# Optimization experiments

Hardware: AMD Instinct MI355X
Metric: run time of the kernel (lower is better)

The kernel has to match this reference:

```python
import jax, jax.numpy as jnp
import numpy as np

N_ITERS = 150   # unrolled projected-subgradient iterations of the convex DRO program
LR0 = 0.05      # initial step size (decays as 1/sqrt(k))


def project_simplex(v):
    """Euclidean projection of v onto the probability simplex {z >= 0, sum z = 1}."""
    n = v.shape[0]
    u = jnp.sort(v)[::-1]
    css = jnp.cumsum(u)
    idx = jnp.arange(1, n + 1, dtype=v.dtype)
    rho = jnp.sum(u + (1.0 - css) / idx > 0)
    theta = (css[rho - 1] - 1.0) / rho.astype(v.dtype)
    return jnp.maximum(v - theta, 0.0)


def dro_solve(ep, y_hat, delta, gamma):
    """Solve the TV-DRO portfolio problem (Ben-Tal et al. 2013 tractable dual):
        min_{z in simplex, c, eta, lam>=0}
            eta + delta*lam + (1/T) sum_t max(-lam, (ep_t@z - c)^2 - eta) - gamma * y_hat@z
    via unrolled projected subgradient descent (differentiable solver layer).
    """
    n_obs, n_y = ep.shape

    def objective(params):
        z, c, eta, lam = params
        r = ep @ z - c                       # (n_obs,) residual portfolio returns
        m = jnp.maximum(-lam, r * r - eta)   # TV phi-conjugate term
        return eta + delta * lam + jnp.mean(m) - gamma * jnp.dot(y_hat, z)

    grad_fn = jax.grad(objective)
    init = (jnp.full((n_y,), 1.0 / n_y, dtype=ep.dtype),
            jnp.zeros((), ep.dtype), jnp.zeros((), ep.dtype),
            jnp.asarray(0.1, ep.dtype))

    def step(params, k):
        g = grad_fn(params)
        lr = LR0 / jnp.sqrt(1.0 + k)
        z, c, eta, lam = [p - lr * gi for p, gi in zip(params, g)]
        z = project_simplex(z)
        lam = jnp.maximum(lam, 0.0)
        return (z, c, eta, lam), None

    (z, _, _, _), _ = jax.lax.scan(step, init, jnp.arange(N_ITERS, dtype=ep.dtype))
    return z


def setup_inputs() -> dict:
    key = jax.random.key(0)
    k1, k2, k3, k4 = jax.random.split(key, 4)
    n_obs, n_x, n_y = 256, 64, 128
    X = jax.random.normal(k1, (n_obs, n_x), dtype=jnp.float32)
    Y = 0.05 * jax.random.normal(k2, (n_obs, n_y), dtype=jnp.float32)
    W = jax.random.normal(k3, (n_y, n_x), dtype=jnp.float32) / np.sqrt(n_x)
    b = 0.01 * jax.random.normal(k4, (n_y,), dtype=jnp.float32)
    delta = jnp.asarray(0.1, jnp.float32)
    gamma = jnp.asarray(0.1, jnp.float32)
    return {"X": X, "Y": Y, "W": W, "b": b, "delta": delta, "gamma": gamma}


def reference(X, Y, W, b, delta, gamma):
    Y_hat = X @ W.T + b            # pred_layer applied to each x_t (batched)
    ep = Y - Y_hat                 # (n_obs, n_y) residuals
    # One DRO solve per scenario y_hat_t, all sharing the same residual matrix ep.
    Z_star = jax.vmap(lambda yh: dro_solve(ep, yh, delta, gamma))(Y_hat)
    return Z_star, Y_hat
```

## Files before the change

### kernel.cpp

```cpp
#include <hip/hip_runtime.h>
#include <math.h>

#define T_OBS 256
#define NY 128
#define NITER 150

#define DPP_ROW_SHR1 0x111
#define DPP_ROW_SHR2 0x112
#define DPP_ROW_SHR4 0x114
#define DPP_ROW_SHR8 0x118
#define DPP_BCAST15  0x142
#define DPP_BCAST31  0x143

#define DPP_ADD_F32(x, ctrl) \
    (x) += __int_as_float(__builtin_amdgcn_update_dpp(0, __float_as_int(x), (ctrl), 0xf, 0xf, true))

__device__ __forceinline__ void wave_sum2(float& a, float& b) {
    DPP_ADD_F32(a, DPP_ROW_SHR1); DPP_ADD_F32(b, DPP_ROW_SHR1);
    DPP_ADD_F32(a, DPP_ROW_SHR2); DPP_ADD_F32(b, DPP_ROW_SHR2);
    DPP_ADD_F32(a, DPP_ROW_SHR4); DPP_ADD_F32(b, DPP_ROW_SHR4);
    DPP_ADD_F32(a, DPP_ROW_SHR8); DPP_ADD_F32(b, DPP_ROW_SHR8);
    DPP_ADD_F32(a, DPP_BCAST15);  DPP_ADD_F32(b, DPP_BCAST15);
    DPP_ADD_F32(a, DPP_BCAST31);  DPP_ADD_F32(b, DPP_BCAST31);
    a = __int_as_float(__builtin_amdgcn_readlane(__float_as_int(a), 63));
    b = __int_as_float(__builtin_amdgcn_readlane(__float_as_int(b), 63));
}

__device__ __forceinline__ float rl(float x, int l) {
    return __int_as_float(__builtin_amdgcn_readlane(__float_as_int(x), l));
}

__global__ __launch_bounds__(128)
void pred_kernel(const float* __restrict__ X, const float* __restrict__ Y,
                 const float* __restrict__ W, const float* __restrict__ b,
                 float* __restrict__ yhat, float* __restrict__ ep) {
    __shared__ float xrow[64];
    const int t = blockIdx.x;
    const int j = threadIdx.x;
    if (j < 64) xrow[j] = X[t * 64 + j];
    __syncthreads();
    const float* wr = W + j * 64;
    float acc = 0.f;
#pragma unroll
    for (int x = 0; x < 64; ++x) acc = fmaf(xrow[x], wr[x], acc);
    const float yh = acc + b[j];
    yhat[t * NY + j] = yh;
    ep[t * NY + j] = Y[t * NY + j] - yh;
}

__global__ __launch_bounds__(256, 1)
void dro_kernel(const float* __restrict__ ep_g, const float* __restrict__ yhat_g,
                float* __restrict__ z_out,
                const float* __restrict__ d_delta, const float* __restrict__ d_gamma) {
    __shared__ float gzp[2][4][NY];
    __shared__ __align__(16) float red[2][8];

    const int tid  = threadIdx.x;
    const int lane = tid & 63;
    const int wid  = tid >> 6;
    const int blk  = blockIdx.x;

    float4 rA[32];
    {
        const float4* eg4 = (const float4*)ep_g + tid * 32;
#pragma unroll
        for (int q = 0; q < 32; ++q) rA[q] = eg4[q];
    }

    const int j0    = lane << 1;
    const int tbase = wid << 6;
    float2 rB[64];
#pragma unroll
    for (int tt = 0; tt < 64; ++tt)
        rB[tt] = *(const float2*)(ep_g + (tbase + tt) * NY + j0);

    const float yh0 = yhat_g[blk * NY + j0];
    const float yh1 = yhat_g[blk * NY + j0 + 1];

    float z0 = 1.0f / 128.0f, z1 = 1.0f / 128.0f;
    float act0 = 1.f, act1 = 1.f;

    const float delta = d_delta[0];
    const float gamma = d_gamma[0];
    float c = 0.f, eta = 0.f, lam = 0.1f;
    int buf = 0;

    for (int k = 0; k < NITER; ++k) {
        const float lr = 0.05f * __builtin_amdgcn_rsqf(1.0f + (float)k);

        float a0 = 0.f, a1 = 0.f, a2 = 0.f, a3 = 0.f;
#pragma unroll
        for (int q = 0; q < 32; ++q) {
            const float4 e = rA[q];
            const float za = rl(z0, 2 * q);
            const float zb = rl(z1, 2 * q);
            const float zc = rl(z0, 2 * q + 1);
            const float zd = rl(z1, 2 * q + 1);
            a0 = fmaf(e.x, za, a0);
            a1 = fmaf(e.y, zb, a1);
            a2 = fmaf(e.z, zc, a2);
            a3 = fmaf(e.w, zd, a3);
        }
        const float r  = (a0 + a1) + (a2 + a3) - c;
        const float q2 = r * r - eta;
        const float aa = -lam;
        const float st = (q2 > aa) ? 1.0f : ((q2 == aa) ? 0.5f : 0.0f);
        const float wv = st * r;

        float s1 = st, s2 = wv;
        wave_sum2(s1, s2);
        if (lane == 0) { red[buf][wid * 2] = s1; red[buf][wid * 2 + 1] = s2; }

        float p0 = 0.f, p1 = 0.f, p2 = 0.f, p3 = 0.f;
#pragma unroll
        for (int tt = 0; tt < 64; tt += 2) {
            const float wa = rl(wv, tt);
            const float wb = rl(wv, tt + 1);
            const float2 ea = rB[tt];
            const float2 eb = rB[tt + 1];
            p0 = fmaf(wa, ea.x, p0);
            p1 = fmaf(wa, ea.y, p1);
            p2 = fmaf(wb, eb.x, p2);
            p3 = fmaf(wb, eb.y, p3);
        }
        *(float2*)&gzp[buf][wid][j0] = make_float2(p0 + p2, p1 + p3);

        __syncthreads();

        const float4 rd0 = *(const float4*)&red[buf][0];
        const float4 rd1 = *(const float4*)&red[buf][4];
        const float S1 = (rd0.x + rd0.z) + (rd1.x + rd1.z);
        const float S2 = (rd0.y + rd0.w) + (rd1.y + rd1.w);
        c   -= lr * (-(2.0f / 256.0f) * S2);
        eta -= lr * (1.0f - S1 * (1.0f / 256.0f));
        lam  = fmaxf(lam - lr * (delta - 1.0f + S1 * (1.0f / 256.0f)), 0.0f);

        const float2 g0v = *(const float2*)&gzp[buf][0][j0];
        const float2 g1v = *(const float2*)&gzp[buf][1][j0];
        const float2 g2v = *(const float2*)&gzp[buf][2][j0];
        const float2 g3v = *(const float2*)&gzp[buf][3][j0];
        const float g0 = (g0v.x + g1v.x) + (g2v.x + g3v.x);
        const float g1 = (g0v.y + g1v.y) + (g2v.y + g3v.y);
        const float v0 = z0 - lr * ((2.0f / 256.0f) * g0 - gamma * yh0);
        const float v1 = z1 - lr * ((2.0f / 256.0f) * g1 - gamma * yh1);

        float theta = 0.f;
        for (int attempt = 0; attempt < 2; ++attempt) {
            for (int m = 0; m < 128; ++m) {
                float s  = act0 * v0 + act1 * v1;
                float cc = act0 + act1;
                wave_sum2(s, cc);
                theta = (s - 1.0f) * __builtin_amdgcn_rcpf(cc);
                const float n0 = (v0 > theta) ? act0 : 0.f;
                const float n1 = (v1 > theta) ? act1 : 0.f;
                const bool changed = (n0 != act0) || (n1 != act1);
                act0 = n0; act1 = n1;
                if (!__any(changed)) break;
            }
            const bool viol = ((act0 == 0.f) && (v0 > theta)) ||
                              ((act1 == 0.f) && (v1 > theta));
            if (!__any(viol)) break;
            act0 = 1.f; act1 = 1.f;
        }
        z0 = fmaxf(v0 - theta, 0.f);
        z1 = fmaxf(v1 - theta, 0.f);

        buf ^= 1;
    }

    if (wid == 0) *(float2*)&z_out[blk * NY + j0] = make_float2(z0, z1);
}

extern "C" void kernel_launch(void* const* d_in, const int* in_sizes, int n_in,
                              void* d_out, int out_size, void* d_ws, size_t ws_size,
                              hipStream_t stream) {
    const float* X       = (const float*)d_in[0];
    const float* Y       = (const float*)d_in[1];
    const float* W       = (const float*)d_in[2];
    const float* b       = (const float*)d_in[3];
    const float* d_delta = (const float*)d_in[4];
    const float* d_gamma = (const float*)d_in[5];

    float* z_out    = (float*)d_out;
    float* yhat_out = z_out + T_OBS * NY;
    float* ep_ws    = (float*)d_ws;

    pred_kernel<<<T_OBS, 128, 0, stream>>>(X, Y, W, b, yhat_out, ep_ws);
    dro_kernel<<<T_OBS, 256, 0, stream>>>(ep_ws, yhat_out, z_out, d_delta, d_gamma);
}
```

Measured before the change: 238.7 us.

## Split DRO solve across 512 threads with halved per-thread register tiles

Doubles the DRO block size from 256 to 512 threads. Each observation row's ep@z dot product is split in half across two threads, and the halves are combined through LDS. The gradient reduction over observations now spans 8 waves of 32 rows each, with the redundant wave sums scaled by 0.5. The aim is to halve per-thread serial work and register tiles so more waves run per CU. The cost is an extra __syncthreads per iteration and more LDS traffic, and the simplex projection is now computed redundantly by all 8 waves.

```diff
diff --git a/kernel.cpp b/kernel.cpp
--- a/kernel.cpp
+++ b/kernel.cpp
@@ -48,31 +48,35 @@
     ep[t * NY + j] = Y[t * NY + j] - yh;
 }
 
-__global__ __launch_bounds__(256, 1)
+__global__ __launch_bounds__(512, 2)
 void dro_kernel(const float* __restrict__ ep_g, const float* __restrict__ yhat_g,
                 float* __restrict__ z_out,
                 const float* __restrict__ d_delta, const float* __restrict__ d_gamma) {
-    __shared__ float gzp[2][4][NY];
-    __shared__ __align__(16) float red[2][8];
+    __shared__ __align__(16) float part_lds[T_OBS * 2];
+    __shared__ __align__(16) float gz_f[8 * 130];
+    __shared__ __align__(16) float red_s[16];
 
     const int tid  = threadIdx.x;
     const int lane = tid & 63;
     const int wid  = tid >> 6;
     const int blk  = blockIdx.x;
-
-    float4 rA[32];
+    const int h    = tid >> 8;
+    const int trow = tid & 255;
+    const int m    = lane & 31;
+    const int prow = wid * 32 + m;
+    const int j0   = lane << 1;
+
+    float4 rA[16];
     {
-        const float4* eg4 = (const float4*)ep_g + tid * 32;
-#pragma unroll
-        for (int q = 0; q < 32; ++q) rA[q] = eg4[q];
+        const float4* eg4 = (const float4*)ep_g + trow * 32 + h * 16;
+#pragma unroll
+        for (int q = 0; q < 16; ++q) rA[q] = eg4[q];
     }
 
-    const int j0    = lane << 1;
-    const int tbase = wid << 6;
-    float2 rB[64];
-#pragma unroll
-    for (int tt = 0; tt < 64; ++tt)
-        rB[tt] = *(const float2*)(ep_g + (tbase + tt) * NY + j0);
+    float2 rB[32];
+#pragma unroll
+    for (int tt = 0; tt < 32; ++tt)
+        rB[tt] = *(const float2*)(ep_g + (wid * 32 + tt) * NY + j0);
 
     const float yh0 = yhat_g[blk * NY + j0];
     const float yh1 = yhat_g[blk * NY + j0 + 1];
@@ -83,25 +87,31 @@
     const float delta = d_delta[0];
     const float gamma = d_gamma[0];
     float c = 0.f, eta = 0.f, lam = 0.1f;
-    int buf = 0;
+
+    const int zlb = h << 5;
 
     for (int k = 0; k < NITER; ++k) {
         const float lr = 0.05f * __builtin_amdgcn_rsqf(1.0f + (float)k);
 
         float a0 = 0.f, a1 = 0.f, a2 = 0.f, a3 = 0.f;
 #pragma unroll
-        for (int q = 0; q < 32; ++q) {
+        for (int q = 0; q < 16; ++q) {
             const float4 e = rA[q];
-            const float za = rl(z0, 2 * q);
-            const float zb = rl(z1, 2 * q);
-            const float zc = rl(z0, 2 * q + 1);
-            const float zd = rl(z1, 2 * q + 1);
+            const float za = rl(z0, zlb + 2 * q);
+            const float zb = rl(z1, zlb + 2 * q);
+            const float zc = rl(z0, zlb + 2 * q + 1);
+            const float zd = rl(z1, zlb + 2 * q + 1);
             a0 = fmaf(e.x, za, a0);
             a1 = fmaf(e.y, zb, a1);
             a2 = fmaf(e.z, zc, a2);
             a3 = fmaf(e.w, zd, a3);
         }
-        const float r  = (a0 + a1) + (a2 + a3) - c;
+        part_lds[trow * 2 + h] = (a0 + a1) + (a2 + a3);
+
+        __syncthreads();
+
+        const float2 pp = *(const float2*)&part_lds[prow * 2];
+        const float r  = (pp.x + pp.y) - c;
         const float q2 = r * r - eta;
         const float aa = -lam;
         const float st = (q2 > aa) ? 1.0f : ((q2 == aa) ? 0.5f : 0.0f);
@@ -109,11 +119,11 @@
 
         float s1 = st, s2 = wv;
         wave_sum2(s1, s2);
-        if (lane == 0) { red[buf][wid * 2] = s1; red[buf][wid * 2 + 1] = s2; }
+        if (lane == 0) { red_s[wid * 2] = s1; red_s[wid * 2 + 1] = s2; }
 
         float p0 = 0.f, p1 = 0.f, p2 = 0.f, p3 = 0.f;
 #pragma unroll
-        for (int tt = 0; tt < 64; tt += 2) {
+        for (int tt = 0; tt < 32; tt += 2) {
             const float wa = rl(wv, tt);
             const float wb = rl(wv, tt + 1);
             const float2 ea = rB[tt];
@@ -123,30 +133,35 @@
             p2 = fmaf(wb, eb.x, p2);
             p3 = fmaf(wb, eb.y, p3);
         }
-        *(float2*)&gzp[buf][wid][j0] = make_float2(p0 + p2, p1 + p3);
+        *(float2*)&gz_f[wid * 130 + j0] = make_float2(p0 + p2, p1 + p3);
 
         __syncthreads();
 
-        const float4 rd0 = *(const float4*)&red[buf][0];
-        const float4 rd1 = *(const float4*)&red[buf][4];
-        const float S1 = (rd0.x + rd0.z) + (rd1.x + rd1.z);
-        const float S2 = (rd0.y + rd0.w) + (rd1.y + rd1.w);
+        const float4 rd0 = *(const float4*)&red_s[0];
+        const float4 rd1 = *(const float4*)&red_s[4];
+        const float4 rd2 = *(const float4*)&red_s[8];
+        const float4 rd3 = *(const float4*)&red_s[12];
+        const float S1 = 0.5f * (((rd0.x + rd0.z) + (rd1.x + rd1.z)) +
+                                 ((rd2.x + rd2.z) + (rd3.x + rd3.z)));
+        const float S2 = 0.5f * (((rd0.y + rd0.w) + (rd1.y + rd1.w)) +
+                                 ((rd2.y + rd2.w) + (rd3.y + rd3.w)));
         c   -= lr * (-(2.0f / 256.0f) * S2);
         eta -= lr * (1.0f - S1 * (1.0f / 256.0f));
         lam  = fmaxf(lam - lr * (delta - 1.0f + S1 * (1.0f / 256.0f)), 0.0f);
 
-        const float2 g0v = *(const float2*)&gzp[buf][0][j0];
-        const float2 g1v = *(const float2*)&gzp[buf][1][j0];
-        const float2 g2v = *(const float2*)&gzp[buf][2][j0];
-        const float2 g3v = *(const float2*)&gzp[buf][3][j0];
-        const float g0 = (g0v.x + g1v.x) + (g2v.x + g3v.x);
-        const float g1 = (g0v.y + g1v.y) + (g2v.y + g3v.y);
+        float g0 = 0.f, g1 = 0.f;
+#pragma unroll
+        for (int w = 0; w < 8; ++w) {
+            const float2 gw = *(const float2*)&gz_f[w * 130 + j0];
+            g0 += gw.x;
+            g1 += gw.y;
+        }
         const float v0 = z0 - lr * ((2.0f / 256.0f) * g0 - gamma * yh0);
         const float v1 = z1 - lr * ((2.0f / 256.0f) * g1 - gamma * yh1);
 
         float theta = 0.f;
         for (int attempt = 0; attempt < 2; ++attempt) {
-            for (int m = 0; m < 128; ++m) {
+            for (int it = 0; it < 128; ++it) {
                 float s  = act0 * v0 + act1 * v1;
                 float cc = act0 + act1;
                 wave_sum2(s, cc);
@@ -164,8 +179,6 @@
         }
         z0 = fmaxf(v0 - theta, 0.f);
         z1 = fmaxf(v1 - theta, 0.f);
-
-        buf ^= 1;
     }
 
     if (wid == 0) *(float2*)&z_out[blk * NY + j0] = make_float2(z0, z1);
@@ -186,5 +199,5 @@
     float* ep_ws    = (float*)d_ws;
 
     pred_kernel<<<T_OBS, 128, 0, stream>>>(X, Y, W, b, yhat_out, ep_ws);
-    dro_kernel<<<T_OBS, 256, 0, stream>>>(ep_ws, yhat_out, z_out, d_delta, d_gamma);
-}
+    dro_kernel<<<T_OBS, 512, 0, stream>>>(ep_ws, yhat_out, z_out, d_delta, d_gamma);
+}
```

After: 316.4 us. 1.33x slower.

## Broadcast z and weights via per-wave LDS and use packed FP32 FMAs

Applied to the files above, without the earlier changes.

The two per-iteration matvecs no longer broadcast z and the residual weights one lane at a time with readlane. Each wave now writes them to a private LDS row and reads them back as float4 broadcasts, then accumulates with v_pk_fma_f32 inline asm that does two FMAs per instruction. This targets the serial readlane/SALU-to-VALU traffic and halves the FMA instruction count. In exchange it adds LDS round trips with no extra barriers, relying on each wave reading only its own row, plus empty asm pins that force the register-resident ep copies to stay in VGPRs.

```diff
diff --git a/kernel.cpp b/kernel.cpp
--- a/kernel.cpp
+++ b/kernel.cpp
@@ -4,6 +4,8 @@
 #define T_OBS 256
 #define NY 128
 #define NITER 150
+
+typedef float f2 __attribute__((ext_vector_type(2)));
 
 #define DPP_ROW_SHR1 0x111
 #define DPP_ROW_SHR2 0x112
@@ -26,8 +28,8 @@
     b = __int_as_float(__builtin_amdgcn_readlane(__float_as_int(b), 63));
 }
 
-__device__ __forceinline__ float rl(float x, int l) {
-    return __int_as_float(__builtin_amdgcn_readlane(__float_as_int(x), l));
+__device__ __forceinline__ void pk_fma(f2& acc, f2 a, f2 b) {
+    asm("v_pk_fma_f32 %0, %1, %2, %0" : "+v"(acc) : "v"(a), "v"(b));
 }
 
 __global__ __launch_bounds__(128)
@@ -52,27 +54,39 @@
 void dro_kernel(const float* __restrict__ ep_g, const float* __restrict__ yhat_g,
                 float* __restrict__ z_out,
                 const float* __restrict__ d_delta, const float* __restrict__ d_gamma) {
-    __shared__ float gzp[2][4][NY];
-    __shared__ __align__(16) float red[2][8];
+    __shared__ __align__(16) float z_lds[4][NY];
+    __shared__ __align__(16) float wdup[4][NY];
+    __shared__ __align__(16) float gzp[2][4][NY];
+    __shared__ __align__(16) float red_s[2][8];
 
     const int tid  = threadIdx.x;
     const int lane = tid & 63;
     const int wid  = tid >> 6;
     const int blk  = blockIdx.x;
-
-    float4 rA[32];
+    const int j0   = lane << 1;
+    const int tbase = wid << 6;
+
+    f2 rA2[64];
     {
         const float4* eg4 = (const float4*)ep_g + tid * 32;
 #pragma unroll
-        for (int q = 0; q < 32; ++q) rA[q] = eg4[q];
+        for (int q = 0; q < 32; ++q) {
+            const float4 t4 = eg4[q];
+            f2 lo; lo.x = t4.x; lo.y = t4.y;
+            f2 hi; hi.x = t4.z; hi.y = t4.w;
+            rA2[2 * q] = lo; rA2[2 * q + 1] = hi;
+        }
     }
 
-    const int j0    = lane << 1;
-    const int tbase = wid << 6;
-    float2 rB[64];
+    f2 rB[64];
 #pragma unroll
     for (int tt = 0; tt < 64; ++tt)
-        rB[tt] = *(const float2*)(ep_g + (tbase + tt) * NY + j0);
+        rB[tt] = *(const f2*)(ep_g + (tbase + tt) * NY + j0);
+
+#pragma unroll
+    for (int i = 0; i < 64; ++i) asm volatile("" : "+v"(rA2[i]));
+#pragma unroll
+    for (int i = 0; i < 64; ++i) asm volatile("" : "+v"(rB[i]));
 
     const float yh0 = yhat_g[blk * NY + j0];
     const float yh1 = yhat_g[blk * NY + j0 + 1];
@@ -85,23 +99,25 @@
     float c = 0.f, eta = 0.f, lam = 0.1f;
     int buf = 0;
 
+    { f2 zi; zi.x = z0; zi.y = z1; *(f2*)&z_lds[wid][j0] = zi; }
+
     for (int k = 0; k < NITER; ++k) {
         const float lr = 0.05f * __builtin_amdgcn_rsqf(1.0f + (float)k);
 
-        float a0 = 0.f, a1 = 0.f, a2 = 0.f, a3 = 0.f;
-#pragma unroll
-        for (int q = 0; q < 32; ++q) {
-            const float4 e = rA[q];
-            const float za = rl(z0, 2 * q);
-            const float zb = rl(z1, 2 * q);
-            const float zc = rl(z0, 2 * q + 1);
-            const float zd = rl(z1, 2 * q + 1);
-            a0 = fmaf(e.x, za, a0);
-            a1 = fmaf(e.y, zb, a1);
-            a2 = fmaf(e.z, zc, a2);
-            a3 = fmaf(e.w, zd, a3);
-        }
-        const float r  = (a0 + a1) + (a2 + a3) - c;
+        f2 accA; accA.x = 0.f; accA.y = 0.f;
+        f2 accB; accB.x = 0.f; accB.y = 0.f;
+        {
+            const float4* zl = (const float4*)&z_lds[wid][0];
+#pragma unroll
+            for (int q = 0; q < 32; ++q) {
+                const float4 z4 = zl[q];
+                f2 zlo; zlo.x = z4.x; zlo.y = z4.y;
+                f2 zhi; zhi.x = z4.z; zhi.y = z4.w;
+                pk_fma(accA, rA2[2 * q], zlo);
+                pk_fma(accB, rA2[2 * q + 1], zhi);
+            }
+        }
+        const float r  = (accA.x + accA.y) + (accB.x + accB.y) - c;
         const float q2 = r * r - eta;
         const float aa = -lam;
         const float st = (q2 > aa) ? 1.0f : ((q2 == aa) ? 0.5f : 0.0f);
@@ -109,36 +125,38 @@
 
         float s1 = st, s2 = wv;
         wave_sum2(s1, s2);
-        if (lane == 0) { red[buf][wid * 2] = s1; red[buf][wid * 2 + 1] = s2; }
-
-        float p0 = 0.f, p1 = 0.f, p2 = 0.f, p3 = 0.f;
-#pragma unroll
-        for (int tt = 0; tt < 64; tt += 2) {
-            const float wa = rl(wv, tt);
-            const float wb = rl(wv, tt + 1);
-            const float2 ea = rB[tt];
-            const float2 eb = rB[tt + 1];
-            p0 = fmaf(wa, ea.x, p0);
-            p1 = fmaf(wa, ea.y, p1);
-            p2 = fmaf(wb, eb.x, p2);
-            p3 = fmaf(wb, eb.y, p3);
-        }
-        *(float2*)&gzp[buf][wid][j0] = make_float2(p0 + p2, p1 + p3);
+        if (lane == 0) { red_s[buf][wid * 2] = s1; red_s[buf][wid * 2 + 1] = s2; }
+
+        { f2 wd; wd.x = wv; wd.y = wv; *(f2*)&wdup[wid][j0] = wd; }
+        f2 pP; pP.x = 0.f; pP.y = 0.f;
+        f2 pQ; pQ.x = 0.f; pQ.y = 0.f;
+        {
+            const float4* wl = (const float4*)&wdup[wid][0];
+#pragma unroll
+            for (int tt = 0; tt < 64; tt += 2) {
+                const float4 w4 = wl[tt >> 1];
+                f2 wa; wa.x = w4.x; wa.y = w4.y;
+                f2 wb; wb.x = w4.z; wb.y = w4.w;
+                pk_fma(pP, rB[tt], wa);
+                pk_fma(pQ, rB[tt + 1], wb);
+            }
+        }
+        { f2 gp; gp.x = pP.x + pQ.x; gp.y = pP.y + pQ.y; *(f2*)&gzp[buf][wid][j0] = gp; }
 
         __syncthreads();
 
-        const float4 rd0 = *(const float4*)&red[buf][0];
-        const float4 rd1 = *(const float4*)&red[buf][4];
+        const float4 rd0 = *(const float4*)&red_s[buf][0];
+        const float4 rd1 = *(const float4*)&red_s[buf][4];
         const float S1 = (rd0.x + rd0.z) + (rd1.x + rd1.z);
         const float S2 = (rd0.y + rd0.w) + (rd1.y + rd1.w);
         c   -= lr * (-(2.0f / 256.0f) * S2);
         eta -= lr * (1.0f - S1 * (1.0f / 256.0f));
         lam  = fmaxf(lam - lr * (delta - 1.0f + S1 * (1.0f / 256.0f)), 0.0f);
 
-        const float2 g0v = *(const float2*)&gzp[buf][0][j0];
-        const float2 g1v = *(const float2*)&gzp[buf][1][j0];
-        const float2 g2v = *(const float2*)&gzp[buf][2][j0];
-        const float2 g3v = *(const float2*)&gzp[buf][3][j0];
+        const f2 g0v = *(const f2*)&gzp[buf][0][j0];
+        const f2 g1v = *(const f2*)&gzp[buf][1][j0];
+        const f2 g2v = *(const f2*)&gzp[buf][2][j0];
+        const f2 g3v = *(const f2*)&gzp[buf][3][j0];
         const float g0 = (g0v.x + g1v.x) + (g2v.x + g3v.x);
         const float g1 = (g0v.y + g1v.y) + (g2v.y + g3v.y);
         const float v0 = z0 - lr * ((2.0f / 256.0f) * g0 - gamma * yh0);
@@ -165,10 +183,12 @@
         z0 = fmaxf(v0 - theta, 0.f);
         z1 = fmaxf(v1 - theta, 0.f);
 
+        { f2 zn; zn.x = z0; zn.y = z1; *(f2*)&z_lds[wid][j0] = zn; }
+
         buf ^= 1;
     }
 
-    if (wid == 0) *(float2*)&z_out[blk * NY + j0] = make_float2(z0, z1);
+    if (wid == 0) { f2 zo; zo.x = z0; zo.y = z1; *(f2*)&z_out[blk * NY + j0] = zo; }
 }
 
 extern "C" void kernel_launch(void* const* d_in, const int* in_sizes, int n_in,
```

Result: slower. 288.6 us (+20.9%).
